# Performance work log

Measured on AMD Instinct MI355X. Metric: run time of the kernel, lower is better.

Reference implementation:

```python
import jax, jax.numpy as jnp
import numpy as np

ALPHA = 0.2        # LeakyReLU negative slope
OUT_FEATURE = 256
NEG_INF = -1e9


def setup_inputs() -> dict:
    key = jax.random.key(0)
    k1, k2, k3, k4 = jax.random.split(key, 4)
    N, F_IN, F_OUT = 8192, 512, OUT_FEATURE
    x = jax.random.normal(k1, (N, F_IN), dtype=jnp.float32)
    adj = jax.random.randint(k2, (N, N), 0, 2, dtype=jnp.int32)
    # Xavier-uniform-ish params
    W = jax.random.normal(k3, (F_IN, F_OUT), dtype=jnp.float32) * (1.414 / np.sqrt(F_IN))
    a = jax.random.normal(k4, (2 * F_OUT, 1), dtype=jnp.float32) * (1.414 / np.sqrt(2 * F_OUT))
    return {"x": x, "adj": adj, "W": W, "a": a}


def reference(x, adj, W, a):
    # x: [N, F_in], adj: [N, N] int, W: [F_in, F_out], a: [2*F_out, 1]
    h = x @ W                                   # [N, F_out]
    a_src = a[:OUT_FEATURE, 0]                  # [F_out]
    a_dst = a[OUT_FEATURE:, 0]                  # [F_out]
    e_i = h @ a_src                             # [N]
    e_j = h @ a_dst                             # [N]
    e = e_i[:, None] + e_j[None, :]             # [N, N] additive scores
    e = jnp.where(e > 0, e, ALPHA * e)          # LeakyReLU
    e = jnp.where(adj <= 0, NEG_INF, e)         # mask non-edges
    attn = jax.nn.softmax(e, axis=-1)           # row-wise softmax
    out = attn @ h                              # [N, F_out] aggregate
    return jax.nn.elu(out)                      # dropout is identity in eval
```

## Files before the change

### kernel.cpp

```cpp
#include <hip/hip_runtime.h>
#include <hip/hip_fp16.h>

#define N_NODES 8192
#define F_IN    512
#define F_OUT   256
#define LOG2E   1.4426950408889634f

typedef __attribute__((ext_vector_type(8))) _Float16 half8;
typedef __attribute__((ext_vector_type(2))) __fp16   fp16x2;
typedef __attribute__((ext_vector_type(4))) float    f32x4;
typedef __attribute__((ext_vector_type(4))) int      i32x4;

union H8U4 { half8 h; uint4 u; };
union H2U  { fp16x2 h; unsigned u; };

__global__ __launch_bounds__(256) void k_prep(const float* __restrict__ W,
                                              unsigned short* __restrict__ wph,
                                              unsigned short* __restrict__ wpl,
                                              unsigned* __restrict__ emax_u) {
  const int gid = blockIdx.x * 256 + threadIdx.x;
  if (gid == 0) *emax_u = 0u;
  const int k = gid >> 8;
  const int c = gid & 255;
  const float w = W[(size_t)k * F_OUT + c];
  const _Float16 hi = (_Float16)w;
  const _Float16 lo = (_Float16)(w - (float)hi);
  const size_t idx =
      (((size_t)(k >> 5) * 16 + (c >> 4)) * 64 + (c & 15) + 16 * ((k >> 3) & 3)) * 8 +
      (k & 7);
  wph[idx] = *(const unsigned short*)&hi;
  wpl[idx] = *(const unsigned short*)&lo;
}

__global__ __launch_bounds__(512) void k_hgemm(const float* __restrict__ x,
                                               const uint4* __restrict__ wph4,
                                               const uint4* __restrict__ wpl4,
                                               const float* __restrict__ a,
                                               unsigned short* __restrict__ hpack,
                                               float* __restrict__ EI,
                                               float* __restrict__ EJ,
                                               unsigned* __restrict__ emax_u) {
  __shared__ float eip[4][32], ejp[4][32], emx[32];
  const int r0   = blockIdx.x * 32;
  const int tid  = threadIdx.x;
  const int wid  = tid >> 6, lane = tid & 63;
  const int mg   = wid >> 2, ng = wid & 3;
  const int lo16 = lane & 15, hi4 = lane >> 4;

  const float* xrow = x + (size_t)(r0 + mg * 16 + lo16) * F_IN + hi4 * 8;
  const uint4* whb = wph4 + (size_t)(ng * 4) * 64 + lane;
  const uint4* wlb = wpl4 + (size_t)(ng * 4) * 64 + lane;

  f32x4 acc[4] = {};

  float4 xa = *(const float4*)(xrow);
  float4 xb = *(const float4*)(xrow + 4);
  uint4 wh[4], wl[4];
#pragma unroll
  for (int nf = 0; nf < 4; ++nf) {
    wh[nf] = whb[(size_t)nf * 64];
    wl[nf] = wlb[(size_t)nf * 64];
  }

#pragma unroll
  for (int ks = 0; ks < 16; ++ks) {
    H8U4 ah, al;
    const float v[8] = {xa.x, xa.y, xa.z, xa.w, xb.x, xb.y, xb.z, xb.w};
#pragma unroll
    for (int j = 0; j < 8; ++j) {
      const _Float16 h = (_Float16)v[j];
      ah.h[j] = h;
      al.h[j] = (_Float16)(v[j] - (float)h);
    }
    if (ks + 1 < 16) {
      xa = *(const float4*)(xrow + (ks + 1) * 32);
      xb = *(const float4*)(xrow + (ks + 1) * 32 + 4);
    }
#pragma unroll
    for (int nf = 0; nf < 4; ++nf) {
      H8U4 bh, bl;
      bh.u = wh[nf];
      bl.u = wl[nf];
      acc[nf] = __builtin_amdgcn_mfma_f32_16x16x32_f16(ah.h, bh.h, acc[nf], 0, 0, 0);
      acc[nf] = __builtin_amdgcn_mfma_f32_16x16x32_f16(al.h, bh.h, acc[nf], 0, 0, 0);
      acc[nf] = __builtin_amdgcn_mfma_f32_16x16x32_f16(ah.h, bl.h, acc[nf], 0, 0, 0);
    }
    if (ks + 1 < 16) {
#pragma unroll
      for (int nf = 0; nf < 4; ++nf) {
        wh[nf] = whb[(size_t)((ks + 1) * 16 + nf) * 64];
        wl[nf] = wlb[(size_t)((ks + 1) * 16 + nf) * 64];
      }
    }
  }

  float asv[4], adv[4];
#pragma unroll
  for (int nf = 0; nf < 4; ++nf) {
    const int c = ng * 64 + nf * 16 + lo16;
    asv[nf] = a[c];
    adv[nf] = a[F_OUT + c];
  }
#pragma unroll
  for (int q = 0; q < 4; ++q) {
    float s1 = acc[0][q] * asv[0] + acc[1][q] * asv[1] + acc[2][q] * asv[2] +
               acc[3][q] * asv[3];
    float s2 = acc[0][q] * adv[0] + acc[1][q] * adv[1] + acc[2][q] * adv[2] +
               acc[3][q] * adv[3];
#pragma unroll
    for (int o = 1; o < 16; o <<= 1) {
      s1 += __shfl_xor(s1, o);
      s2 += __shfl_xor(s2, o);
    }
    if (lo16 == 0) {
      const int rl = mg * 16 + hi4 * 4 + q;
      eip[ng][rl] = s1;
      ejp[ng][rl] = s2;
    }
  }

#pragma unroll
  for (int nf = 0; nf < 4; ++nf) {
#pragma unroll
    for (int q = 0; q < 4; ++q) {
      const int row = r0 + mg * 16 + hi4 * 4 + q;
      const int col = ng * 64 + nf * 16 + lo16;
      const size_t idx =
          (((size_t)(row >> 5) * 16 + (col >> 4)) * 64 + (col & 15) +
           16 * ((row >> 3) & 3)) * 8 + (row & 7);
      const _Float16 hv = (_Float16)acc[nf][q];
      hpack[idx] = *(const unsigned short*)&hv;
    }
  }

  __syncthreads();
  if (tid < 32) {
    const float s1 = eip[0][tid] + eip[1][tid] + eip[2][tid] + eip[3][tid];
    const float s2 = ejp[0][tid] + ejp[1][tid] + ejp[2][tid] + ejp[3][tid];
    const int row = r0 + tid;
    EI[row] = s1 * LOG2E;
    const float e2 = s2 * LOG2E;
    EJ[row] = e2;
    emx[tid] = e2;
  }
  __syncthreads();
  if (tid == 0) {
    float m = emx[0];
#pragma unroll
    for (int i = 1; i < 32; ++i) m = fmaxf(m, emx[i]);
    unsigned b = __float_as_uint(m);
    unsigned u = (b & 0x80000000u) ? ~b : (b | 0x80000000u);
    atomicMax(emax_u, u);
  }
}

__global__ __launch_bounds__(512, 4) void k_pv(const int* __restrict__ adj,
                                               const uint4* __restrict__ hp4,
                                               const float* __restrict__ EI,
                                               const float* __restrict__ EJ,
                                               const unsigned* __restrict__ emax_u,
                                               float* __restrict__ npart,
                                               float* __restrict__ dpart,
                                               int ntiles) {
  __shared__ __align__(16) uint4 ps4[8 * 64];
  __shared__ float ejhi[2048], ejlo[2048];
  __shared__ float A1[64], A2[64], den[64];
  const int rowbase = blockIdx.x * 64;
  const int split   = blockIdx.y;
  const int jt0     = split * ntiles;
  const int tid     = threadIdx.x;
  const int wid  = tid >> 6, lane = tid & 63;
  const int lo   = lane & 15, hi = lane >> 4;

  float EMAX;
  {
    const unsigned u = *emax_u;
    EMAX = (u & 0x80000000u) ? __uint_as_float(u & 0x7fffffffu) : __uint_as_float(~u);
  }
  if (tid < 64) {
    const float e  = EI[rowbase + tid];
    const float s  = e + EMAX;
    const float mi = fmaxf(s, 0.2f * s);
    A1[tid] = e - mi;
    A2[tid] = 0.2f * e - mi;
    den[tid] = 0.f;
  }
  const bool uselds = (ntiles <= 32);
  if (uselds) {
    int eidx = jt0 * 64 + tid * 4;
    if (eidx > N_NODES - 4) eidx = N_NODES - 4;
    const float4 ev = *(const float4*)&EJ[eidx];
    *(float4*)&ejhi[tid * 4] = ev;
    float4 el = {0.2f * ev.x, 0.2f * ev.y, 0.2f * ev.z, 0.2f * ev.w};
    *(float4*)&ejlo[tid * 4] = el;
  }
  __syncthreads();

  const int msub = wid & 3, ksw = wid >> 2;
  const int row_p = msub * 16 + lo;
  const int jloc  = ksw * 32 + hi * 8;
  const float a1r = A1[row_p], a2r = A2[row_p];
  const int*   adjp = adj + (size_t)(rowbase + row_p) * N_NODES + jt0 * 64 + jloc;
  const float* ejg  = EJ + jt0 * 64 + jloc;
  const int mg = wid >> 2, ng = wid & 3;
  const uint4* hb = hp4 + (ng * 4) * 64 + lane;

  f32x4 acc[2][4] = {};
  float dacc = 0.f;

  i32x4 cur0 = __builtin_nontemporal_load((const i32x4*)(adjp));
  i32x4 cur1 = __builtin_nontemporal_load((const i32x4*)(adjp + 4));
  i32x4 nxt0 = {0, 0, 0, 0}, nxt1 = {0, 0, 0, 0};
  if (ntiles > 1) {
    nxt0 = __builtin_nontemporal_load((const i32x4*)(adjp + 64));
    nxt1 = __builtin_nontemporal_load((const i32x4*)(adjp + 68));
  }

  for (int jt = 0; jt < ntiles; ++jt) {
    const int tb = (jt0 + jt) * 2048;
    const uint4 b00 = hb[tb + 0 * 1024 + 0 * 64];
    const uint4 b01 = hb[tb + 0 * 1024 + 1 * 64];
    const uint4 b02 = hb[tb + 0 * 1024 + 2 * 64];
    const uint4 b03 = hb[tb + 0 * 1024 + 3 * 64];
    const uint4 b10 = hb[tb + 1 * 1024 + 0 * 64];
    const uint4 b11 = hb[tb + 1 * 1024 + 1 * 64];
    const uint4 b12 = hb[tb + 1 * 1024 + 2 * 64];
    const uint4 b13 = hb[tb + 1 * 1024 + 3 * 64];

    float eh[8], el[8];
    if (uselds) {
      const float4 h0 = *(const float4*)&ejhi[jt * 64 + jloc];
      const float4 h1 = *(const float4*)&ejhi[jt * 64 + jloc + 4];
      const float4 l0 = *(const float4*)&ejlo[jt * 64 + jloc];
      const float4 l1 = *(const float4*)&ejlo[jt * 64 + jloc + 4];
      eh[0]=h0.x; eh[1]=h0.y; eh[2]=h0.z; eh[3]=h0.w;
      eh[4]=h1.x; eh[5]=h1.y; eh[6]=h1.z; eh[7]=h1.w;
      el[0]=l0.x; el[1]=l0.y; el[2]=l0.z; el[3]=l0.w;
      el[4]=l1.x; el[5]=l1.y; el[6]=l1.z; el[7]=l1.w;
    } else {
      const float4 e0 = *(const float4*)(ejg + jt * 64);
      const float4 e1 = *(const float4*)(ejg + jt * 64 + 4);
      eh[0]=e0.x; eh[1]=e0.y; eh[2]=e0.z; eh[3]=e0.w;
      eh[4]=e1.x; eh[5]=e1.y; eh[6]=e1.z; eh[7]=e1.w;
#pragma unroll
      for (int j = 0; j < 8; ++j) el[j] = 0.2f * eh[j];
    }
    const int am[8] = {cur0.x, cur0.y, cur0.z, cur0.w, cur1.x, cur1.y, cur1.z, cur1.w};
    float ph[8];
#pragma unroll
    for (int j = 0; j < 8; ++j) {
      const float s = fmaxf(eh[j] + a1r, el[j] + a2r);
      const float p = __builtin_amdgcn_exp2f(s);
      ph[j] = (am[j] > 0) ? p : 0.f;
    }
    dacc += ((ph[0] + ph[1]) + (ph[2] + ph[3])) + ((ph[4] + ph[5]) + (ph[6] + ph[7]));
    H2U q0, q1, q2, q3;
    q0.h = __builtin_amdgcn_cvt_pkrtz(ph[0], ph[1]);
    q1.h = __builtin_amdgcn_cvt_pkrtz(ph[2], ph[3]);
    q2.h = __builtin_amdgcn_cvt_pkrtz(ph[4], ph[5]);
    q3.h = __builtin_amdgcn_cvt_pkrtz(ph[6], ph[7]);
    uint4 pk = {q0.u, q1.u, q2.u, q3.u};

    asm volatile("" ::: "memory");
    __builtin_amdgcn_s_barrier();
    asm volatile("" ::: "memory");
    ps4[wid * 64 + lane] = pk;
    cur0 = nxt0; cur1 = nxt1;
    if (jt + 2 < ntiles) {
      const int* ap = adjp + (jt + 2) * 64;
      nxt0 = __builtin_nontemporal_load((const i32x4*)ap);
      nxt1 = __builtin_nontemporal_load((const i32x4*)(ap + 4));
    }
    asm volatile("s_waitcnt lgkmcnt(0)" ::: "memory");
    __builtin_amdgcn_s_barrier();
    asm volatile("" ::: "memory");

    H8U4 a00, a01, a10, a11;
    a00.u = ps4[(0 * 4 + mg * 2 + 0) * 64 + lane];
    a10.u = ps4[(0 * 4 + mg * 2 + 1) * 64 + lane];
    a01.u = ps4[(1 * 4 + mg * 2 + 0) * 64 + lane];
    a11.u = ps4[(1 * 4 + mg * 2 + 1) * 64 + lane];
    H8U4 b;
    __builtin_amdgcn_s_setprio(1);
    b.u = b00;
    acc[0][0] = __builtin_amdgcn_mfma_f32_16x16x32_f16(a00.h, b.h, acc[0][0], 0, 0, 0);
    acc[1][0] = __builtin_amdgcn_mfma_f32_16x16x32_f16(a10.h, b.h, acc[1][0], 0, 0, 0);
    b.u = b01;
    acc[0][1] = __builtin_amdgcn_mfma_f32_16x16x32_f16(a00.h, b.h, acc[0][1], 0, 0, 0);
    acc[1][1] = __builtin_amdgcn_mfma_f32_16x16x32_f16(a10.h, b.h, acc[1][1], 0, 0, 0);
    b.u = b02;
    acc[0][2] = __builtin_amdgcn_mfma_f32_16x16x32_f16(a00.h, b.h, acc[0][2], 0, 0, 0);
    acc[1][2] = __builtin_amdgcn_mfma_f32_16x16x32_f16(a10.h, b.h, acc[1][2], 0, 0, 0);
    b.u = b03;
    acc[0][3] = __builtin_amdgcn_mfma_f32_16x16x32_f16(a00.h, b.h, acc[0][3], 0, 0, 0);
    acc[1][3] = __builtin_amdgcn_mfma_f32_16x16x32_f16(a10.h, b.h, acc[1][3], 0, 0, 0);
    b.u = b10;
    acc[0][0] = __builtin_amdgcn_mfma_f32_16x16x32_f16(a01.h, b.h, acc[0][0], 0, 0, 0);
    acc[1][0] = __builtin_amdgcn_mfma_f32_16x16x32_f16(a11.h, b.h, acc[1][0], 0, 0, 0);
    b.u = b11;
    acc[0][1] = __builtin_amdgcn_mfma_f32_16x16x32_f16(a01.h, b.h, acc[0][1], 0, 0, 0);
    acc[1][1] = __builtin_amdgcn_mfma_f32_16x16x32_f16(a11.h, b.h, acc[1][1], 0, 0, 0);
    b.u = b12;
    acc[0][2] = __builtin_amdgcn_mfma_f32_16x16x32_f16(a01.h, b.h, acc[0][2], 0, 0, 0);
    acc[1][2] = __builtin_amdgcn_mfma_f32_16x16x32_f16(a11.h, b.h, acc[1][2], 0, 0, 0);
    b.u = b13;
    acc[0][3] = __builtin_amdgcn_mfma_f32_16x16x32_f16(a01.h, b.h, acc[0][3], 0, 0, 0);
    acc[1][3] = __builtin_amdgcn_mfma_f32_16x16x32_f16(a11.h, b.h, acc[1][3], 0, 0, 0);
    __builtin_amdgcn_s_setprio(0);
  }

  atomicAdd(&den[row_p], dacc);
  __syncthreads();

  float* npb = npart + (size_t)split * N_NODES * F_OUT;
#pragma unroll
  for (int mi_ = 0; mi_ < 2; ++mi_) {
    const int rb = rowbase + (mg * 2 + mi_) * 16 + hi * 4;
#pragma unroll
    for (int nf = 0; nf < 4; ++nf) {
      const int col = ng * 64 + nf * 16 + lo;
#pragma unroll
      for (int r2 = 0; r2 < 4; ++r2)
        __builtin_nontemporal_store(acc[mi_][nf][r2],
                                    &npb[(size_t)(rb + r2) * F_OUT + col]);
    }
  }
  if (tid < 64)
    __builtin_nontemporal_store(den[tid],
                                &dpart[(size_t)split * N_NODES + rowbase + tid]);
}

__global__ __launch_bounds__(256) void k_fin(const float* __restrict__ npart,
                                             const float* __restrict__ dpart,
                                             float* __restrict__ out,
                                             int nsplit) {
  const int gid = blockIdx.x * 256 + threadIdx.x;
  const int row = gid >> 6;
  const int c4  = (gid & 63) << 2;
  f32x4 s = {0.f, 0.f, 0.f, 0.f};
  float d = 0.f;
  for (int sp = 0; sp < nsplit; ++sp) {
    const f32x4 v = __builtin_nontemporal_load(
        (const f32x4*)(npart + ((size_t)sp * N_NODES + row) * F_OUT + c4));
    s += v;
    d += dpart[(size_t)sp * N_NODES + row];
  }
  const float inv = 1.f / d;
  float o[4] = {s.x * inv, s.y * inv, s.z * inv, s.w * inv};
#pragma unroll
  for (int i = 0; i < 4; ++i) o[i] = (o[i] > 0.f) ? o[i] : expm1f(o[i]);
  float4 ov = {o[0], o[1], o[2], o[3]};
  *(float4*)(out + (size_t)row * F_OUT + c4) = ov;
}

extern "C" void kernel_launch(void* const* d_in, const int* in_sizes, int n_in,
                              void* d_out, int out_size, void* d_ws, size_t ws_size,
                              hipStream_t stream) {
  const float* x   = (const float*)d_in[0];
  const int*   adj = (const int*)d_in[1];
  const float* W   = (const float*)d_in[2];
  const float* a   = (const float*)d_in[3];
  float* out = (float*)d_out;
  char*  ws  = (char*)d_ws;

  unsigned short* hpack = (unsigned short*)ws;
  size_t off = (size_t)4 * 1024 * 1024;
  float* EI = (float*)(ws + off); off += (size_t)N_NODES * 4;
  float* EJ = (float*)(ws + off); off += (size_t)N_NODES * 4;
  unsigned* emax_u = (unsigned*)(ws + off); off += 256;
  float* dpart = (float*)(ws + off); off += (size_t)8 * N_NODES * 4;
  unsigned short* wph = (unsigned short*)(ws + off); off += (size_t)F_IN * F_OUT * 2;
  unsigned short* wpl = (unsigned short*)(ws + off); off += (size_t)F_IN * F_OUT * 2;
  float* npart = (float*)(ws + off);

  int nsplit = 4;
  while (nsplit > 1 && off + (size_t)nsplit * N_NODES * F_OUT * 4 > ws_size) nsplit >>= 1;

  k_prep<<<dim3((F_IN * F_OUT) / 256), dim3(256), 0, stream>>>(W, wph, wpl, emax_u);
  k_hgemm<<<dim3(N_NODES / 32), dim3(512), 0, stream>>>(
      x, (const uint4*)wph, (const uint4*)wpl, a, hpack, EI, EJ, emax_u);
  k_pv<<<dim3(128, nsplit), dim3(512), 0, stream>>>(adj, (const uint4*)hpack, EI, EJ,
                                                    emax_u, npart, dpart, 128 / nsplit);
  k_fin<<<dim3(N_NODES * 64 / 256), dim3(256), 0, stream>>>(npart, dpart, out, nsplit);
}
```

Measured before the change: 148.7 us.

## Stage h tiles into double-buffered LDS via global_load_lds and prefetch EJ

Instead of each wave loading its B fragments of h directly from global memory every tile, the block cooperatively copies each 2048-uint4 tile of h into a double-buffered LDS area with global_load_lds, one tile ahead, and waits with explicit vmcnt counts before the barrier. The EJ LDS cache and its precomputed 0.2 scaling are replaced by register prefetch of EJ two tiles ahead, with the 0.2 multiply done inline. The aim is to cut redundant global/L2 reads of h across waves and hide load latency behind the softmax/MFMA work. The cost is 64KB of LDS per block, which may cut occupancy under launch_bounds(512,4), and the hand-coded vmcnt values must match the exact number of outstanding loads.

```diff
diff --git a/kernel.cpp b/kernel.cpp
--- a/kernel.cpp
+++ b/kernel.cpp
@@ -13,6 +13,13 @@
 
 union H8U4 { half8 h; uint4 u; };
 union H2U  { fp16x2 h; unsigned u; };
+
+#define AS1 __attribute__((address_space(1)))
+#define AS3 __attribute__((address_space(3)))
+
+static __device__ __forceinline__ void glds16(const uint4* g, uint4* l) {
+  __builtin_amdgcn_global_load_lds((const AS1 void*)g, (AS3 void*)l, 16, 0, 0);
+}
 
 __global__ __launch_bounds__(256) void k_prep(const float* __restrict__ W,
                                               unsigned short* __restrict__ wph,
@@ -163,7 +170,7 @@
                                                float* __restrict__ dpart,
                                                int ntiles) {
   __shared__ __align__(16) uint4 ps4[8 * 64];
-  __shared__ float ejhi[2048], ejlo[2048];
+  __shared__ __align__(16) uint4 bs[2][2048];
   __shared__ float A1[64], A2[64], den[64];
   const int rowbase = blockIdx.x * 64;
   const int split   = blockIdx.y;
@@ -185,71 +192,53 @@
     A2[tid] = 0.2f * e - mi;
     den[tid] = 0.f;
   }
-  const bool uselds = (ntiles <= 32);
-  if (uselds) {
-    int eidx = jt0 * 64 + tid * 4;
-    if (eidx > N_NODES - 4) eidx = N_NODES - 4;
-    const float4 ev = *(const float4*)&EJ[eidx];
-    *(float4*)&ejhi[tid * 4] = ev;
-    float4 el = {0.2f * ev.x, 0.2f * ev.y, 0.2f * ev.z, 0.2f * ev.w};
-    *(float4*)&ejlo[tid * 4] = el;
-  }
-  __syncthreads();
 
   const int msub = wid & 3, ksw = wid >> 2;
   const int row_p = msub * 16 + lo;
   const int jloc  = ksw * 32 + hi * 8;
-  const float a1r = A1[row_p], a2r = A2[row_p];
   const int*   adjp = adj + (size_t)(rowbase + row_p) * N_NODES + jt0 * 64 + jloc;
   const float* ejg  = EJ + jt0 * 64 + jloc;
   const int mg = wid >> 2, ng = wid & 3;
-  const uint4* hb = hp4 + (ng * 4) * 64 + lane;
 
   f32x4 acc[2][4] = {};
   float dacc = 0.f;
 
+  auto stageB = [&](int tile) {
+    const uint4* gb = hp4 + (size_t)(jt0 + tile) * 2048;
+    uint4* lb = &bs[tile & 1][0];
+#pragma unroll
+    for (int c = 0; c < 4; ++c) {
+      const int s0 = (c * 8 + wid) * 64;
+      glds16(gb + s0 + lane, lb + s0);
+    }
+  };
+
+  stageB(0);
   i32x4 cur0 = __builtin_nontemporal_load((const i32x4*)(adjp));
   i32x4 cur1 = __builtin_nontemporal_load((const i32x4*)(adjp + 4));
   i32x4 nxt0 = {0, 0, 0, 0}, nxt1 = {0, 0, 0, 0};
+  float4 ejc0 = *(const float4*)(ejg);
+  float4 ejc1 = *(const float4*)(ejg + 4);
+  float4 ejn0 = {0, 0, 0, 0}, ejn1 = {0, 0, 0, 0};
   if (ntiles > 1) {
     nxt0 = __builtin_nontemporal_load((const i32x4*)(adjp + 64));
     nxt1 = __builtin_nontemporal_load((const i32x4*)(adjp + 68));
-  }
+    ejn0 = *(const float4*)(ejg + 64);
+    ejn1 = *(const float4*)(ejg + 68);
+  }
+  __syncthreads();
+
+  const float a1r = A1[row_p], a2r = A2[row_p];
 
   for (int jt = 0; jt < ntiles; ++jt) {
-    const int tb = (jt0 + jt) * 2048;
-    const uint4 b00 = hb[tb + 0 * 1024 + 0 * 64];
-    const uint4 b01 = hb[tb + 0 * 1024 + 1 * 64];
-    const uint4 b02 = hb[tb + 0 * 1024 + 2 * 64];
-    const uint4 b03 = hb[tb + 0 * 1024 + 3 * 64];
-    const uint4 b10 = hb[tb + 1 * 1024 + 0 * 64];
-    const uint4 b11 = hb[tb + 1 * 1024 + 1 * 64];
-    const uint4 b12 = hb[tb + 1 * 1024 + 2 * 64];
-    const uint4 b13 = hb[tb + 1 * 1024 + 3 * 64];
-
-    float eh[8], el[8];
-    if (uselds) {
-      const float4 h0 = *(const float4*)&ejhi[jt * 64 + jloc];
-      const float4 h1 = *(const float4*)&ejhi[jt * 64 + jloc + 4];
-      const float4 l0 = *(const float4*)&ejlo[jt * 64 + jloc];
-      const float4 l1 = *(const float4*)&ejlo[jt * 64 + jloc + 4];
-      eh[0]=h0.x; eh[1]=h0.y; eh[2]=h0.z; eh[3]=h0.w;
-      eh[4]=h1.x; eh[5]=h1.y; eh[6]=h1.z; eh[7]=h1.w;
-      el[0]=l0.x; el[1]=l0.y; el[2]=l0.z; el[3]=l0.w;
-      el[4]=l1.x; el[5]=l1.y; el[6]=l1.z; el[7]=l1.w;
-    } else {
-      const float4 e0 = *(const float4*)(ejg + jt * 64);
-      const float4 e1 = *(const float4*)(ejg + jt * 64 + 4);
-      eh[0]=e0.x; eh[1]=e0.y; eh[2]=e0.z; eh[3]=e0.w;
-      eh[4]=e1.x; eh[5]=e1.y; eh[6]=e1.z; eh[7]=e1.w;
-#pragma unroll
-      for (int j = 0; j < 8; ++j) el[j] = 0.2f * eh[j];
-    }
+    float eh[8];
+    eh[0]=ejc0.x; eh[1]=ejc0.y; eh[2]=ejc0.z; eh[3]=ejc0.w;
+    eh[4]=ejc1.x; eh[5]=ejc1.y; eh[6]=ejc1.z; eh[7]=ejc1.w;
     const int am[8] = {cur0.x, cur0.y, cur0.z, cur0.w, cur1.x, cur1.y, cur1.z, cur1.w};
     float ph[8];
 #pragma unroll
     for (int j = 0; j < 8; ++j) {
-      const float s = fmaxf(eh[j] + a1r, el[j] + a2r);
+      const float s = fmaxf(eh[j] + a1r, 0.2f * eh[j] + a2r);
       const float p = __builtin_amdgcn_exp2f(s);
       ph[j] = (am[j] > 0) ? p : 0.f;
     }
@@ -265,13 +254,24 @@
     __builtin_amdgcn_s_barrier();
     asm volatile("" ::: "memory");
     ps4[wid * 64 + lane] = pk;
-    cur0 = nxt0; cur1 = nxt1;
+
+    if (jt + 1 < ntiles) stageB(jt + 1);
+    cur0 = nxt0; cur1 = nxt1; ejc0 = ejn0; ejc1 = ejn1;
     if (jt + 2 < ntiles) {
       const int* ap = adjp + (jt + 2) * 64;
       nxt0 = __builtin_nontemporal_load((const i32x4*)ap);
       nxt1 = __builtin_nontemporal_load((const i32x4*)(ap + 4));
-    }
+      ejn0 = *(const float4*)(ejg + (jt + 2) * 64);
+      ejn1 = *(const float4*)(ejg + (jt + 2) * 64 + 4);
+    }
+
     asm volatile("s_waitcnt lgkmcnt(0)" ::: "memory");
+    if (jt + 1 < ntiles) {
+      if (jt + 2 < ntiles) asm volatile("s_waitcnt vmcnt(12)" ::: "memory");
+      else                 asm volatile("s_waitcnt vmcnt(8)"  ::: "memory");
+    } else {
+      asm volatile("s_waitcnt vmcnt(0)" ::: "memory");
+    }
     __builtin_amdgcn_s_barrier();
     asm volatile("" ::: "memory");
 
@@ -280,30 +280,31 @@
     a10.u = ps4[(0 * 4 + mg * 2 + 1) * 64 + lane];
     a01.u = ps4[(1 * 4 + mg * 2 + 0) * 64 + lane];
     a11.u = ps4[(1 * 4 + mg * 2 + 1) * 64 + lane];
+    const uint4* bb = &bs[jt & 1][(ng * 4) * 64 + lane];
     H8U4 b;
     __builtin_amdgcn_s_setprio(1);
-    b.u = b00;
+    b.u = bb[0 * 1024 + 0 * 64];
     acc[0][0] = __builtin_amdgcn_mfma_f32_16x16x32_f16(a00.h, b.h, acc[0][0], 0, 0, 0);
     acc[1][0] = __builtin_amdgcn_mfma_f32_16x16x32_f16(a10.h, b.h, acc[1][0], 0, 0, 0);
-    b.u = b01;
+    b.u = bb[0 * 1024 + 1 * 64];
     acc[0][1] = __builtin_amdgcn_mfma_f32_16x16x32_f16(a00.h, b.h, acc[0][1], 0, 0, 0);
     acc[1][1] = __builtin_amdgcn_mfma_f32_16x16x32_f16(a10.h, b.h, acc[1][1], 0, 0, 0);
-    b.u = b02;
+    b.u = bb[0 * 1024 + 2 * 64];
     acc[0][2] = __builtin_amdgcn_mfma_f32_16x16x32_f16(a00.h, b.h, acc[0][2], 0, 0, 0);
     acc[1][2] = __builtin_amdgcn_mfma_f32_16x16x32_f16(a10.h, b.h, acc[1][2], 0, 0, 0);
-    b.u = b03;
+    b.u = bb[0 * 1024 + 3 * 64];
     acc[0][3] = __builtin_amdgcn_mfma_f32_16x16x32_f16(a00.h, b.h, acc[0][3], 0, 0, 0);
     acc[1][3] = __builtin_amdgcn_mfma_f32_16x16x32_f16(a10.h, b.h, acc[1][3], 0, 0, 0);
-    b.u = b10;
+    b.u = bb[1 * 1024 + 0 * 64];
     acc[0][0] = __builtin_amdgcn_mfma_f32_16x16x32_f16(a01.h, b.h, acc[0][0], 0, 0, 0);
     acc[1][0] = __builtin_amdgcn_mfma_f32_16x16x32_f16(a11.h, b.h, acc[1][0], 0, 0, 0);
-    b.u = b11;
+    b.u = bb[1 * 1024 + 1 * 64];
     acc[0][1] = __builtin_amdgcn_mfma_f32_16x16x32_f16(a01.h, b.h, acc[0][1], 0, 0, 0);
     acc[1][1] = __builtin_amdgcn_mfma_f32_16x16x32_f16(a11.h, b.h, acc[1][1], 0, 0, 0);
-    b.u = b12;
+    b.u = bb[1 * 1024 + 2 * 64];
     acc[0][2] = __builtin_amdgcn_mfma_f32_16x16x32_f16(a01.h, b.h, acc[0][2], 0, 0, 0);
     acc[1][2] = __builtin_amdgcn_mfma_f32_16x16x32_f16(a11.h, b.h, acc[1][2], 0, 0, 0);
-    b.u = b13;
+    b.u = bb[1 * 1024 + 3 * 64];
     acc[0][3] = __builtin_amdgcn_mfma_f32_16x16x32_f16(a01.h, b.h, acc[0][3], 0, 0, 0);
     acc[1][3] = __builtin_amdgcn_mfma_f32_16x16x32_f16(a11.h, b.h, acc[1][3], 0, 0, 0);
     __builtin_amdgcn_s_setprio(0);
```

Measured after the change: 154.2 us. 3.6% more time.

## Compress adjacency into a bitmask in a separate pass before the attention kernel

Applied to the files above, without the earlier changes.

Adds a streaming kernel that reads the int32 adjacency matrix once and packs it into a 1-bit-per-edge mask using wavefront ballots. The main attention/aggregation kernel then loads one byte of mask per lane per tile instead of two 16-byte int vectors. The goal is to separate the bandwidth-heavy read of the full adjacency from the compute-heavy exp and MFMA loop, which cuts that loop's memory pressure and register use. The cost is an extra kernel launch, an extra 8 MB write and read, and the full adjacency read still remains.

```diff
diff --git a/kernel.cpp b/kernel.cpp
--- a/kernel.cpp
+++ b/kernel.cpp
@@ -9,10 +9,37 @@
 typedef __attribute__((ext_vector_type(8))) _Float16 half8;
 typedef __attribute__((ext_vector_type(2))) __fp16   fp16x2;
 typedef __attribute__((ext_vector_type(4))) float    f32x4;
-typedef __attribute__((ext_vector_type(4))) int      i32x4;
 
 union H8U4 { half8 h; uint4 u; };
 union H2U  { fp16x2 h; unsigned u; };
+
+__global__ __launch_bounds__(256) void k_badj(const int* __restrict__ adj,
+                                              unsigned long long* __restrict__ bm) {
+  const int nw   = (gridDim.x * 256) >> 6;
+  const int gw   = (blockIdx.x * 256 + threadIdx.x) >> 6;
+  const int lane = threadIdx.x & 63;
+  const int nchunk = N_NODES * (N_NODES / 64);
+  for (int c0 = gw * 4; c0 < nchunk; c0 += nw * 4) {
+    const size_t base = (size_t)c0 * 64 + lane;
+    const int v0 = __builtin_nontemporal_load(adj + base);
+    const int v1 = __builtin_nontemporal_load(adj + base + 64);
+    const int v2 = __builtin_nontemporal_load(adj + base + 128);
+    const int v3 = __builtin_nontemporal_load(adj + base + 192);
+    const unsigned long long m0 = __ballot(v0 > 0);
+    const unsigned long long m1 = __ballot(v1 > 0);
+    const unsigned long long m2 = __ballot(v2 > 0);
+    const unsigned long long m3 = __ballot(v3 > 0);
+    if (lane == 0) {
+      uint4 s0, s1;
+      s0.x = (unsigned)m0; s0.y = (unsigned)(m0 >> 32);
+      s0.z = (unsigned)m1; s0.w = (unsigned)(m1 >> 32);
+      s1.x = (unsigned)m2; s1.y = (unsigned)(m2 >> 32);
+      s1.z = (unsigned)m3; s1.w = (unsigned)(m3 >> 32);
+      *(uint4*)(bm + c0)     = s0;
+      *(uint4*)(bm + c0 + 2) = s1;
+    }
+  }
+}
 
 __global__ __launch_bounds__(256) void k_prep(const float* __restrict__ W,
                                               unsigned short* __restrict__ wph,
@@ -154,7 +181,7 @@
   }
 }
 
-__global__ __launch_bounds__(512, 4) void k_pv(const int* __restrict__ adj,
+__global__ __launch_bounds__(512, 4) void k_pv(const unsigned char* __restrict__ bmask,
                                                const uint4* __restrict__ hp4,
                                                const float* __restrict__ EI,
                                                const float* __restrict__ EJ,
@@ -200,7 +227,8 @@
   const int row_p = msub * 16 + lo;
   const int jloc  = ksw * 32 + hi * 8;
   const float a1r = A1[row_p], a2r = A2[row_p];
-  const int*   adjp = adj + (size_t)(rowbase + row_p) * N_NODES + jt0 * 64 + jloc;
+  const unsigned char* mbp =
+      bmask + (size_t)(rowbase + row_p) * (N_NODES / 8) + (size_t)jt0 * 8 + ksw * 4 + hi;
   const float* ejg  = EJ + jt0 * 64 + jloc;
   const int mg = wid >> 2, ng = wid & 3;
   const uint4* hb = hp4 + (ng * 4) * 64 + lane;
@@ -208,13 +236,8 @@
   f32x4 acc[2][4] = {};
   float dacc = 0.f;
 
-  i32x4 cur0 = __builtin_nontemporal_load((const i32x4*)(adjp));
-  i32x4 cur1 = __builtin_nontemporal_load((const i32x4*)(adjp + 4));
-  i32x4 nxt0 = {0, 0, 0, 0}, nxt1 = {0, 0, 0, 0};
-  if (ntiles > 1) {
-    nxt0 = __builtin_nontemporal_load((const i32x4*)(adjp + 64));
-    nxt1 = __builtin_nontemporal_load((const i32x4*)(adjp + 68));
-  }
+  unsigned mcur = mbp[0];
+  unsigned mnxt = (ntiles > 1) ? (unsigned)mbp[8] : 0u;
 
   for (int jt = 0; jt < ntiles; ++jt) {
     const int tb = (jt0 + jt) * 2048;
@@ -245,13 +268,12 @@
 #pragma unroll
       for (int j = 0; j < 8; ++j) el[j] = 0.2f * eh[j];
     }
-    const int am[8] = {cur0.x, cur0.y, cur0.z, cur0.w, cur1.x, cur1.y, cur1.z, cur1.w};
     float ph[8];
 #pragma unroll
     for (int j = 0; j < 8; ++j) {
       const float s = fmaxf(eh[j] + a1r, el[j] + a2r);
       const float p = __builtin_amdgcn_exp2f(s);
-      ph[j] = (am[j] > 0) ? p : 0.f;
+      ph[j] = (mcur & (1u << j)) ? p : 0.f;
     }
     dacc += ((ph[0] + ph[1]) + (ph[2] + ph[3])) + ((ph[4] + ph[5]) + (ph[6] + ph[7]));
     H2U q0, q1, q2, q3;
@@ -265,12 +287,8 @@
     __builtin_amdgcn_s_barrier();
     asm volatile("" ::: "memory");
     ps4[wid * 64 + lane] = pk;
-    cur0 = nxt0; cur1 = nxt1;
-    if (jt + 2 < ntiles) {
-      const int* ap = adjp + (jt + 2) * 64;
-      nxt0 = __builtin_nontemporal_load((const i32x4*)ap);
-      nxt1 = __builtin_nontemporal_load((const i32x4*)(ap + 4));
-    }
+    mcur = mnxt;
+    if (jt + 2 < ntiles) mnxt = (unsigned)mbp[(jt + 2) * 8];
     asm volatile("s_waitcnt lgkmcnt(0)" ::: "memory");
     __builtin_amdgcn_s_barrier();
     asm volatile("" ::: "memory");
@@ -371,15 +389,19 @@
   float* dpart = (float*)(ws + off); off += (size_t)8 * N_NODES * 4;
   unsigned short* wph = (unsigned short*)(ws + off); off += (size_t)F_IN * F_OUT * 2;
   unsigned short* wpl = (unsigned short*)(ws + off); off += (size_t)F_IN * F_OUT * 2;
+  unsigned long long* bmask = (unsigned long long*)(ws + off);
+  off += (size_t)N_NODES * (N_NODES / 8);
   float* npart = (float*)(ws + off);
 
   int nsplit = 4;
   while (nsplit > 1 && off + (size_t)nsplit * N_NODES * F_OUT * 4 > ws_size) nsplit >>= 1;
 
+  k_badj<<<dim3(2048), dim3(256), 0, stream>>>(adj, bmask);
   k_prep<<<dim3((F_IN * F_OUT) / 256), dim3(256), 0, stream>>>(W, wph, wpl, emax_u);
   k_hgemm<<<dim3(N_NODES / 32), dim3(512), 0, stream>>>(
       x, (const uint4*)wph, (const uint4*)wpl, a, hpack, EI, EJ, emax_u);
-  k_pv<<<dim3(128, nsplit), dim3(512), 0, stream>>>(adj, (const uint4*)hpack, EI, EJ,
-                                                    emax_u, npart, dpart, 128 / nsplit);
+  k_pv<<<dim3(128, nsplit), dim3(512), 0, stream>>>(
+      (const unsigned char*)bmask, (const uint4*)hpack, EI, EJ, emax_u, npart, dpart,
+      128 / nsplit);
   k_fin<<<dim3(N_NODES * 64 / 256), dim3(256), 0, stream>>>(npart, dpart, out, nsplit);
 }
```

Measured after the change: 144.5 us. 2.9% less time.
